# Kernel tuning notes

Measured on AMD Instinct MI355X. Metric: run time of the kernel, lower is better.

The kernel has to match this reference:

```python
import jax, jax.numpy as jnp
import numpy as np

B, L, D, C = 8, 4096, 1024, 64


def setup_inputs() -> dict:
    key = jax.random.key(0)
    ks = jax.random.split(key, 9)
    s = 1.0 / np.sqrt(D)

    def lin(k):
        kw, kb = jax.random.split(k)
        return (jax.random.uniform(kw, (D, D), jnp.float32, -s, s),
                jax.random.uniform(kb, (D,), jnp.float32, -s, s))

    Wq_w, Wq_b = lin(ks[1])
    Wk_w, Wk_b = lin(ks[2])
    Wv_w, Wv_b = lin(ks[3])
    Wo_w, Wo_b = lin(ks[4])
    return {
        "X": jax.random.normal(ks[0], (B, L, D), jnp.float32),
        "chunk": C,
        "Wq_w": Wq_w, "Wq_b": Wq_b,
        "Wk_w": Wk_w, "Wk_b": Wk_b,
        "Wv_w": Wv_w, "Wv_b": Wv_b,
        "Wo_w": Wo_w, "Wo_b": Wo_b,
    }


def _chunk_delta_rule(Q, K, V, beta, Cc):
    # Q,K,V: (B,L,d); beta: (B,L,1); Cc divides L
    Bq, Lq, d = Q.shape
    nc = Lq // Cc
    Q, K, V = (x.reshape(Bq, nc, Cc, d) for x in (Q, K, V))
    beta = beta.reshape(Bq, nc, Cc, 1)
    Kb = K * beta
    Vb = V * beta
    tril_strict = jnp.tril(jnp.ones((Cc, Cc), jnp.float32), -1)
    # masked_fill(triu(diag=0), 0) keeps strictly-lower part
    T = -(Kb @ jnp.swapaxes(K, -1, -2)) * tril_strict  # (B,nc,C,C)
    # forward-substitution inverse of (I - strict_lower); C is small & static
    for i in range(1, Cc):
        T = T.at[:, :, i, :i].add(
            jnp.einsum('bnj,bnjc->bnc', T[:, :, i, :], T[:, :, :, :i]))
    T = T + jnp.eye(Cc, dtype=T.dtype)
    W = T @ Kb  # (B,nc,C,d)
    U = T @ Vb  # (B,nc,C,d)
    tril_incl = jnp.tril(jnp.ones((Cc, Cc), jnp.float32))  # masked_fill(triu(1),0)

    def step(S, xs):
        q, k, w, u0 = xs  # each (B,C,d)
        u = u0 - w @ S
        A = (q @ jnp.swapaxes(k, -1, -2)) * tril_incl  # (B,C,C)
        o = A @ u + q @ S
        return S + jnp.swapaxes(k, -1, -2) @ u, o

    S0 = jnp.zeros((Bq, d, d), Q.dtype)
    xs = tuple(jnp.swapaxes(a, 0, 1) for a in (Q, K, W, U))  # (nc,B,C,d)
    _, O = jax.lax.scan(step, S0, xs)
    return jnp.swapaxes(O, 0, 1).reshape(Bq, Lq, d)


def reference(X, chunk, Wq_w, Wq_b, Wk_w, Wk_b, Wv_w, Wv_b, Wo_w, Wo_b):
    Q = X @ Wq_w.T + Wq_b
    K = X @ Wk_w.T + Wk_b
    V = X @ Wv_w.T + Wv_b
    beta = 1.0 / (jnp.sum(K * K, axis=-1, keepdims=True) + 1e-6)
    O = _chunk_delta_rule(Q, K, V, beta, chunk)
    return O @ Wo_w.T + Wo_b
```

## Files before the change

kernel.cpp:

```cpp
#include <hip/hip_runtime.h>
#include <stdint.h>

typedef unsigned short u16;
typedef __attribute__((ext_vector_type(8))) short short8;
typedef __attribute__((ext_vector_type(4))) float float4_;

#define NB 8
#define LL 4096
#define DD 1024
#define CC 64
#define NCH 64

__device__ __forceinline__ u16 f2bf(float f) {
  union { float f; uint32_t u; } v; v.f = f;
  uint32_t u = v.u;
  return (u16)((u + 0x7fffu + ((u >> 16) & 1u)) >> 16);
}
__device__ __forceinline__ float bf2f(u16 h) {
  union { uint32_t u; float f; } v; v.u = ((uint32_t)h) << 16;
  return v.f;
}
__device__ __forceinline__ float4_ mfma16(short8 a, short8 b, float4_ c) {
  return __builtin_amdgcn_mfma_f32_16x16x32_bf16(a, b, c, 0, 0, 0);
}

__global__ void k_detect(const uint32_t* __restrict__ X, int* __restrict__ flag) {
  if (threadIdx.x == 0 && blockIdx.x == 0) {
    int votes = 0;
    for (int i = 0; i < 64; ++i) {
      uint32_t w = X[i];
      uint32_t e = (w >> 7) & 0xFF;
      votes += (e > 134 || e < 110) ? 1 : 0;
    }
    *flag = (votes < 8) ? 1 : 0;
  }
}

__global__ __launch_bounds__(256) void k_convert(const void* __restrict__ src, u16* __restrict__ dst,
                                                 long n8, const int* __restrict__ flag) {
  long i = (long)blockIdx.x * 256 + threadIdx.x;
  if (i >= n8) return;
  if (*flag) {
    ((short8*)dst)[i] = ((const short8*)src)[i];
  } else {
    const float4_* s = (const float4_*)src;
    float4_ a = s[2 * i], b = s[2 * i + 1];
    short8 o;
#pragma unroll
    for (int j = 0; j < 4; ++j) { o[j] = (short)f2bf(a[j]); o[4 + j] = (short)f2bf(b[j]); }
    ((short8*)dst)[i] = o;
  }
}

template <bool DUAL>
__device__ __forceinline__ void gemm128(const u16* __restrict__ A, const u16* __restrict__ W,
                                        const u16* __restrict__ bias, void* __restrict__ Out,
                                        int m0, int n0, const int* __restrict__ flag) {
  __shared__ __attribute__((aligned(16))) u16 As[128 * 64];
  __shared__ __attribute__((aligned(16))) u16 Bs[128 * 64];
  const int tid = threadIdx.x, lane = tid & 63, wv = tid >> 6;
  float4_ acc[2][8];
#pragma unroll
  for (int i = 0; i < 2; ++i)
#pragma unroll
    for (int j = 0; j < 8; ++j) acc[i][j] = (float4_)0.f;

  for (int kk = 0; kk < DD; kk += 64) {
#pragma unroll
    for (int i = 0; i < 4; ++i) {
      int e = tid + 256 * i;
      int row = e >> 3, col = (e & 7) * 8;
      *(short8*)&As[row * 64 + col] = *(const short8*)(A + (size_t)(m0 + row) * DD + kk + col);
      *(short8*)&Bs[row * 64 + col] = *(const short8*)(W + (size_t)(n0 + row) * DD + kk + col);
    }
    __syncthreads();
#pragma unroll
    for (int ks = 0; ks < 2; ++ks) {
      short8 af[2];
#pragma unroll
      for (int mt = 0; mt < 2; ++mt)
        af[mt] = *(const short8*)&As[(32 * wv + 16 * mt + (lane & 15)) * 64 + ks * 32 + (lane >> 4) * 8];
#pragma unroll
      for (int nt = 0; nt < 8; ++nt) {
        short8 bf = *(const short8*)&Bs[(16 * nt + (lane & 15)) * 64 + ks * 32 + (lane >> 4) * 8];
#pragma unroll
        for (int mt = 0; mt < 2; ++mt) acc[mt][nt] = mfma16(af[mt], bf, acc[mt][nt]);
      }
    }
    __syncthreads();
  }
  const bool obf = DUAL ? (*flag != 0) : true;
#pragma unroll
  for (int mt = 0; mt < 2; ++mt)
#pragma unroll
    for (int nt = 0; nt < 8; ++nt) {
      int rg = m0 + 32 * wv + 16 * mt + ((lane >> 4) << 2);
      int cg = n0 + 16 * nt + (lane & 15);
      float bv = bf2f(bias[cg]);
#pragma unroll
      for (int r = 0; r < 4; ++r) {
        float o = acc[mt][nt][r] + bv;
        if (obf) ((u16*)Out)[(size_t)(rg + r) * DD + cg] = f2bf(o);
        else     ((float*)Out)[(size_t)(rg + r) * DD + cg] = o;
      }
    }
}

__global__ __launch_bounds__(256) void k_gemm_qkv(const u16* __restrict__ X,
    const u16* __restrict__ Wq, const u16* __restrict__ bq,
    const u16* __restrict__ Wk, const u16* __restrict__ bk,
    const u16* __restrict__ Wv, const u16* __restrict__ bv,
    u16* __restrict__ Qo, u16* __restrict__ Ko, u16* __restrict__ Vo) {
  int nb = blockIdx.x;
  int mat = nb >> 3, nt = nb & 7;
  const u16 *W, *bi; u16* O;
  if (mat == 0)      { W = Wq; bi = bq; O = Qo; }
  else if (mat == 1) { W = Wk; bi = bk; O = Ko; }
  else               { W = Wv; bi = bv; O = Vo; }
  gemm128<false>(X, W, bi, O, blockIdx.y * 128, nt * 128, nullptr);
}

__global__ __launch_bounds__(256) void k_gemm_o(const u16* __restrict__ A,
    const u16* __restrict__ Wo, const u16* __restrict__ bo, void* __restrict__ Out,
    const int* __restrict__ flag) {
  gemm128<true>(A, Wo, bo, Out, blockIdx.y * 128, blockIdx.x * 128, flag);
}

__global__ __launch_bounds__(256) void k_prep(const u16* __restrict__ Q, const u16* __restrict__ K,
                                              u16* __restrict__ V ,
                                              u16* __restrict__ Aout, u16* __restrict__ Wall,
                                              u16* __restrict__ KTg) {
  const int ch = blockIdx.x, b = blockIdx.y;
  const size_t row0 = (size_t)b * LL + (size_t)ch * CC;
  const int tid = threadIdx.x, lane = tid & 63, wv = tid >> 6;

  __shared__ __attribute__((aligned(16))) float Gs[64 * 65];
  __shared__ __attribute__((aligned(16))) float Ts[64 * 65];
  __shared__ __attribute__((aligned(16))) u16 Kt[64 * 64];
  __shared__ __attribute__((aligned(16))) u16 Qt[64 * 64];
  __shared__ __attribute__((aligned(16))) u16 T2s[64 * 72];
  __shared__ float betas[64];

  float4_ accG[4], accA[4];
#pragma unroll
  for (int ct = 0; ct < 4; ++ct) { accG[ct] = (float4_)0.f; accA[ct] = (float4_)0.f; }

  for (int kk = 0; kk < DD; kk += 64) {
#pragma unroll
    for (int i = 0; i < 2; ++i) {
      int e = tid + 256 * i;
      int row = e >> 3, col = (e & 7) * 8;
      *(short8*)&Kt[row * 64 + col] = *(const short8*)(K + (row0 + row) * DD + kk + col);
      *(short8*)&Qt[row * 64 + col] = *(const short8*)(Q + (row0 + row) * DD + kk + col);
    }
    __syncthreads();
#pragma unroll
    for (int ks = 0; ks < 2; ++ks) {
      short8 ak = *(const short8*)&Kt[(16 * wv + (lane & 15)) * 64 + ks * 32 + (lane >> 4) * 8];
      short8 aq = *(const short8*)&Qt[(16 * wv + (lane & 15)) * 64 + ks * 32 + (lane >> 4) * 8];
#pragma unroll
      for (int ct = 0; ct < 4; ++ct) {
        short8 bk = *(const short8*)&Kt[(16 * ct + (lane & 15)) * 64 + ks * 32 + (lane >> 4) * 8];
        accG[ct] = mfma16(ak, bk, accG[ct]);
        accA[ct] = mfma16(aq, bk, accA[ct]);
      }
    }
    __syncthreads();
  }
  u16* Abase = Aout + (size_t)(b * NCH + ch) * (CC * CC);
#pragma unroll
  for (int ct = 0; ct < 4; ++ct) {
    int i0 = 16 * wv + ((lane >> 4) << 2);
    int c = 16 * ct + (lane & 15);
#pragma unroll
    for (int r = 0; r < 4; ++r) {
      int i = i0 + r;
      Gs[i * 65 + c] = accG[ct][r];
      Abase[i * 64 + c] = f2bf((c <= i) ? accA[ct][r] : 0.f);
    }
  }
  __syncthreads();
  if (tid < 64) betas[tid] = 1.f / (Gs[tid * 65 + tid] + 1e-6f);
  __syncthreads();
  for (int e = tid; e < 4096; e += 256) {
    int i = e >> 6, c = e & 63;
    Ts[i * 65 + c] = (c < i) ? (-betas[i] * Gs[i * 65 + c]) : 0.f;
  }
  __syncthreads();
  for (int i = 1; i < 64; ++i) {
    float rv = 0.f, acc = 0.f;
    if (tid < 64) {
      rv = Ts[i * 65 + tid];
      for (int j = 1; j < i; ++j) {
        float a = __shfl(rv, j);
        acc += a * Ts[j * 65 + tid];
      }
    }
    __syncthreads();
    if (tid < i) Ts[i * 65 + tid] = rv + acc;
    __syncthreads();
  }
  if (tid < 64) Ts[tid * 65 + tid] += 1.f;
  __syncthreads();
  for (int e = tid; e < 4096; e += 256) {
    int i = e >> 6, j = e & 63;
    T2s[i * 72 + j] = f2bf(Ts[i * 65 + j] * betas[j]);
  }
  __syncthreads();

  u16* KTs = (u16*)Gs;
  u16* VTs = (u16*)Ts;
  for (int kk = 0; kk < DD; kk += 64) {
#pragma unroll
    for (int rep = 0; rep < 2; ++rep) {
      int t = tid >> 2;
      int c0 = (tid & 3) * 8 + rep * 32;
      short8 vv = *(const short8*)(V + (row0 + t) * DD + kk + c0);
      short8 vk = *(const short8*)(K + (row0 + t) * DD + kk + c0);
#pragma unroll
      for (int e = 0; e < 8; ++e) { VTs[(c0 + e) * 72 + t] = (u16)vv[e]; KTs[(c0 + e) * 72 + t] = (u16)vk[e]; }
    }
    __syncthreads();
#pragma unroll
    for (int w2 = 0; w2 < 2; ++w2) {
      int e = tid + 256 * w2;
      int jl = e >> 3, toff = (e & 7) * 8;
      *(short8*)(KTg + ((size_t)b * DD + kk + jl) * LL + (size_t)ch * CC + toff) =
          *(const short8*)&KTs[jl * 72 + toff];
    }
    float4_ accU[4], accW[4];
#pragma unroll
    for (int ct = 0; ct < 4; ++ct) { accU[ct] = (float4_)0.f; accW[ct] = (float4_)0.f; }
#pragma unroll
    for (int ks = 0; ks < 2; ++ks) {
      short8 a2 = *(const short8*)&T2s[(16 * wv + (lane & 15)) * 72 + ks * 32 + (lane >> 4) * 8];
#pragma unroll
      for (int ct = 0; ct < 4; ++ct) {
        short8 bu = *(const short8*)&VTs[(16 * ct + (lane & 15)) * 72 + ks * 32 + (lane >> 4) * 8];
        short8 bw = *(const short8*)&KTs[(16 * ct + (lane & 15)) * 72 + ks * 32 + (lane >> 4) * 8];
        accU[ct] = mfma16(a2, bu, accU[ct]);
        accW[ct] = mfma16(a2, bw, accW[ct]);
      }
    }
#pragma unroll
    for (int ct = 0; ct < 4; ++ct) {
      int i0 = 16 * wv + ((lane >> 4) << 2);
      int c = kk + 16 * ct + (lane & 15);
#pragma unroll
      for (int r = 0; r < 4; ++r) {
        V[(row0 + i0 + r) * DD + c]    = f2bf(accU[ct][r]);
        Wall[(row0 + i0 + r) * DD + c] = f2bf(accW[ct][r]);
      }
    }
    __syncthreads();
  }
}

__global__ __launch_bounds__(256, 1) void k_scan_fused(
    const u16* __restrict__ Q, const u16* __restrict__ Wg, const u16* __restrict__ KTg,
    const u16* __restrict__ U0, const u16* __restrict__ Ag, u16* __restrict__ Og) {
  __shared__ __attribute__((aligned(16))) float S[32 * 1028];
  __shared__ __attribute__((aligned(16))) float u_acc[64 * 33];
  __shared__ __attribute__((aligned(16))) float oq_acc[64 * 33];
  __shared__ __attribute__((aligned(16))) u16 uT[32 * 72];

  const int b = blockIdx.x & 7;
  const int dc0 = (blockIdx.x >> 3) * 32;
  const int tid = threadIdx.x, lane = tid & 63, wv = tid >> 6;
  const int r15 = lane & 15, hi = lane >> 4;
  const int khi = hi * 8;
  const int tI = tid >> 2, cI = (tid & 3) * 8;

  for (int i = tid; i < 32 * 1028; i += 256) S[i] = 0.f;
  __syncthreads();

  for (int ch = 0; ch < NCH; ++ch) {
    const size_t row0 = (size_t)b * LL + (size_t)ch * CC;
    {
      short8 v = *(const short8*)(U0 + (row0 + tI) * DD + dc0 + cI);
#pragma unroll
      for (int e = 0; e < 8; ++e) {
        u_acc[tI * 33 + cI + e]  = bf2f((u16)v[e]);
        oq_acc[tI * 33 + cI + e] = 0.f;
      }
    }
    __syncthreads();
    {
      float4_ up[4][2], qp[4][2];
#pragma unroll
      for (int tt = 0; tt < 4; ++tt)
#pragma unroll
        for (int dt = 0; dt < 2; ++dt) { up[tt][dt] = (float4_)0.f; qp[tt][dt] = (float4_)0.f; }
#pragma unroll 2
      for (int ks = 0; ks < 8; ++ks) {
        const int j0 = wv * 256 + ks * 32 + khi;
        short8 sf[2];
#pragma unroll
        for (int dt = 0; dt < 2; ++dt) {
          const float* sp = &S[(dt * 16 + r15) * 1028 + j0];
          float4_ x0 = *(const float4_*)sp;
          float4_ x1 = *(const float4_*)(sp + 4);
          short8 s;
#pragma unroll
          for (int e = 0; e < 4; ++e) { s[e] = (short)f2bf(x0[e]); s[4 + e] = (short)f2bf(x1[e]); }
          sf[dt] = s;
        }
#pragma unroll
        for (int tt = 0; tt < 4; ++tt) {
          const size_t rbase = (row0 + tt * 16 + r15) * DD + j0;
          short8 wf = *(const short8*)(Wg + rbase);
          short8 qf = *(const short8*)(Q + rbase);
#pragma unroll
          for (int dt = 0; dt < 2; ++dt) {
            up[tt][dt] = mfma16(wf, sf[dt], up[tt][dt]);
            qp[tt][dt] = mfma16(qf, sf[dt], qp[tt][dt]);
          }
        }
      }
#pragma unroll
      for (int tt = 0; tt < 4; ++tt)
#pragma unroll
        for (int dt = 0; dt < 2; ++dt) {
          const int t0 = tt * 16 + hi * 4, dc = dt * 16 + r15;
#pragma unroll
          for (int r = 0; r < 4; ++r) {
            atomicAdd(&u_acc[(t0 + r) * 33 + dc], -up[tt][dt][r]);
            atomicAdd(&oq_acc[(t0 + r) * 33 + dc], qp[tt][dt][r]);
          }
        }
    }
    __syncthreads();
    {
      const float* pu = &u_acc[tI * 33 + cI];
#pragma unroll
      for (int e = 0; e < 8; ++e) uT[(cI + e) * 72 + tI] = f2bf(pu[e]);
    }
    __syncthreads();
    {
      short8 ub[2][2];
#pragma unroll
      for (int dt = 0; dt < 2; ++dt)
#pragma unroll
        for (int ks = 0; ks < 2; ++ks)
          ub[dt][ks] = *(const short8*)&uT[(dt * 16 + r15) * 72 + ks * 32 + khi];
      const size_t ktb = ((size_t)b * DD) * LL + (size_t)ch * CC;
#pragma unroll 4
      for (int djt = 0; djt < 16; ++djt) {
        const int dj0 = wv * 256 + djt * 16;
        short8 kf0 = *(const short8*)(KTg + ktb + (size_t)(dj0 + r15) * LL + khi);
        short8 kf1 = *(const short8*)(KTg + ktb + (size_t)(dj0 + r15) * LL + 32 + khi);
#pragma unroll
        for (int dt = 0; dt < 2; ++dt) {
          float* sp = &S[(dt * 16 + r15) * 1028 + dj0 + hi * 4];
          float4_ c = *(const float4_*)sp;
          c = mfma16(kf0, ub[dt][0], c);
          c = mfma16(kf1, ub[dt][1], c);
          *(float4_*)sp = c;
        }
      }
      const u16* Ab = Ag + (size_t)(b * NCH + ch) * (CC * CC);
      short8 af0 = *(const short8*)(Ab + (wv * 16 + r15) * CC + khi);
      short8 af1 = *(const short8*)(Ab + (wv * 16 + r15) * CC + 32 + khi);
      const int t0 = wv * 16 + hi * 4;
#pragma unroll
      for (int dt = 0; dt < 2; ++dt) {
        const int dc = dt * 16 + r15;
        float4_ c;
#pragma unroll
        for (int r = 0; r < 4; ++r) c[r] = oq_acc[(t0 + r) * 33 + dc];
        c = mfma16(af0, ub[dt][0], c);
        c = mfma16(af1, ub[dt][1], c);
#pragma unroll
        for (int r = 0; r < 4; ++r)
          Og[(row0 + t0 + r) * DD + dc0 + dc] = f2bf(c[r]);
      }
    }
    __syncthreads();
  }
}

extern "C" void kernel_launch(void* const* d_in, const int* in_sizes, int n_in,
                              void* d_out, int out_size, void* d_ws, size_t ws_size,
                              hipStream_t stream) {
  (void)in_sizes; (void)n_in; (void)out_size; (void)ws_size;
  const void* X  = d_in[0];
  const void* Wq = d_in[2]; const void* bq = d_in[3];
  const void* Wk = d_in[4]; const void* bk = d_in[5];
  const void* Wv = d_in[6]; const void* bv = d_in[7];
  const void* Wo = d_in[8]; const void* bo = d_in[9];

  char* ws = (char*)d_ws;
  int* flag = (int*)ws;
  char* p = ws + 256;
  const size_t E2 = (size_t)NB * LL * DD * 2;
  u16* xb   = (u16*)p; p += E2;
  u16* kt   = xb;
  u16* wqb  = (u16*)p; p += (size_t)DD * DD * 2;
  u16* wkb  = (u16*)p; p += (size_t)DD * DD * 2;
  u16* wvb  = (u16*)p; p += (size_t)DD * DD * 2;
  u16* wob  = (u16*)p; p += (size_t)DD * DD * 2;
  u16* bqb  = (u16*)p; p += 4096;
  u16* bkb  = (u16*)p; p += 4096;
  u16* bvb  = (u16*)p; p += 4096;
  u16* bob  = (u16*)p; p += 4096;
  u16* q_ws = (u16*)p; p += E2;
  u16* k_ws = (u16*)p; p += E2;
  u16* v_ws = (u16*)p; p += E2;
  u16* a_ws = (u16*)p; p += (size_t)NB * NCH * CC * CC * 2;
  u16* w_all = (u16*)p; p += E2;

  k_detect<<<1, 64, 0, stream>>>((const uint32_t*)X, flag);
  const long nX = (long)NB * LL * DD / 8;
  k_convert<<<(nX + 255) / 256, 256, 0, stream>>>(X, xb, nX, flag);
  const long nW = (long)DD * DD / 8;
  k_convert<<<(nW + 255) / 256, 256, 0, stream>>>(Wq, wqb, nW, flag);
  k_convert<<<(nW + 255) / 256, 256, 0, stream>>>(Wk, wkb, nW, flag);
  k_convert<<<(nW + 255) / 256, 256, 0, stream>>>(Wv, wvb, nW, flag);
  k_convert<<<(nW + 255) / 256, 256, 0, stream>>>(Wo, wob, nW, flag);
  const long nBias = DD / 8;
  k_convert<<<1, 256, 0, stream>>>(bq, bqb, nBias, flag);
  k_convert<<<1, 256, 0, stream>>>(bk, bkb, nBias, flag);
  k_convert<<<1, 256, 0, stream>>>(bv, bvb, nBias, flag);
  k_convert<<<1, 256, 0, stream>>>(bo, bob, nBias, flag);

  k_gemm_qkv<<<dim3(24, 256), 256, 0, stream>>>(xb, wqb, bqb, wkb, bkb, wvb, bvb, q_ws, k_ws, v_ws);
  k_prep<<<dim3(64, 8), 256, 0, stream>>>(q_ws, k_ws, v_ws, a_ws, w_all, kt);
  k_scan_fused<<<dim3(256), 256, 0, stream>>>(q_ws, w_all, kt, v_ws, a_ws, k_ws);
  k_gemm_o<<<dim3(8, 256), 256, 0, stream>>>(k_ws, wob, bob, d_out, flag);
}
```

Measured before the change: 3.022 ms.

## Double scan block threads, remove uT transpose staging, prefetch next chunk U0

The fused chunk scan kernel now runs 512 threads (8 waves) per block, so each wave handles half the d-range for the S·W/Q products and the S update. The u transpose now goes straight from u_acc into registers with packed bf16 conversion instructions, which removes the uT shared buffer. The next chunk's U0 load and the oq_acc reset are folded into the end of the previous iteration, dropping one barrier per chunk. The output A·u step is split across 8 waves, one tile each. The aim is more latency hiding in the serial scan, at the cost of more register pressure under the 512-thread launch bound and more shared-memory atomic contention.

```diff
diff --git a/kernel.cpp b/kernel.cpp
--- a/kernel.cpp
+++ b/kernel.cpp
@@ -4,6 +4,7 @@
 typedef unsigned short u16;
 typedef __attribute__((ext_vector_type(8))) short short8;
 typedef __attribute__((ext_vector_type(4))) float float4_;
+typedef __attribute__((ext_vector_type(4))) unsigned short us4;
 
 #define NB 8
 #define LL 4096
@@ -23,6 +24,12 @@
 __device__ __forceinline__ float4_ mfma16(short8 a, short8 b, float4_ c) {
   return __builtin_amdgcn_mfma_f32_16x16x32_bf16(a, b, c, 0, 0, 0);
 }
+__device__ __forceinline__ uint32_t cvtpk(float lo, float hi) {
+  uint32_t r;
+  asm("v_cvt_pk_bf16_f32 %0, %1, %2" : "=v"(r) : "v"(lo), "v"(hi));
+  return r;
+}
+union S8U { short8 s; uint32_t w[4]; };
 
 __global__ void k_detect(const uint32_t* __restrict__ X, int* __restrict__ flag) {
   if (threadIdx.x == 0 && blockIdx.x == 0) {
@@ -256,54 +263,54 @@
   }
 }
 
-__global__ __launch_bounds__(256, 1) void k_scan_fused(
+__global__ __launch_bounds__(512, 2) void k_scan_fused(
     const u16* __restrict__ Q, const u16* __restrict__ Wg, const u16* __restrict__ KTg,
     const u16* __restrict__ U0, const u16* __restrict__ Ag, u16* __restrict__ Og) {
   __shared__ __attribute__((aligned(16))) float S[32 * 1028];
   __shared__ __attribute__((aligned(16))) float u_acc[64 * 33];
   __shared__ __attribute__((aligned(16))) float oq_acc[64 * 33];
-  __shared__ __attribute__((aligned(16))) u16 uT[32 * 72];
 
   const int b = blockIdx.x & 7;
   const int dc0 = (blockIdx.x >> 3) * 32;
   const int tid = threadIdx.x, lane = tid & 63, wv = tid >> 6;
   const int r15 = lane & 15, hi = lane >> 4;
   const int khi = hi * 8;
-  const int tI = tid >> 2, cI = (tid & 3) * 8;
-
-  for (int i = tid; i < 32 * 1028; i += 256) S[i] = 0.f;
+  const int tIq = tid >> 3, cIq = (tid & 7) * 4;
+
+  for (int i = tid; i < 32 * 1028; i += 512) S[i] = 0.f;
+  {
+    us4 v = *(const us4*)(U0 + ((size_t)b * LL + tIq) * DD + dc0 + cIq);
+#pragma unroll
+    for (int e = 0; e < 4; ++e) {
+      u_acc[tIq * 33 + cIq + e] = bf2f(v[e]);
+      oq_acc[tIq * 33 + cIq + e] = 0.f;
+    }
+  }
   __syncthreads();
 
   for (int ch = 0; ch < NCH; ++ch) {
     const size_t row0 = (size_t)b * LL + (size_t)ch * CC;
     {
-      short8 v = *(const short8*)(U0 + (row0 + tI) * DD + dc0 + cI);
-#pragma unroll
-      for (int e = 0; e < 8; ++e) {
-        u_acc[tI * 33 + cI + e]  = bf2f((u16)v[e]);
-        oq_acc[tI * 33 + cI + e] = 0.f;
-      }
-    }
-    __syncthreads();
-    {
       float4_ up[4][2], qp[4][2];
 #pragma unroll
       for (int tt = 0; tt < 4; ++tt)
 #pragma unroll
         for (int dt = 0; dt < 2; ++dt) { up[tt][dt] = (float4_)0.f; qp[tt][dt] = (float4_)0.f; }
-#pragma unroll 2
-      for (int ks = 0; ks < 8; ++ks) {
-        const int j0 = wv * 256 + ks * 32 + khi;
+#pragma unroll
+      for (int ks = 0; ks < 4; ++ks) {
+        const int j0 = wv * 128 + ks * 32 + khi;
         short8 sf[2];
 #pragma unroll
         for (int dt = 0; dt < 2; ++dt) {
           const float* sp = &S[(dt * 16 + r15) * 1028 + j0];
           float4_ x0 = *(const float4_*)sp;
           float4_ x1 = *(const float4_*)(sp + 4);
-          short8 s;
-#pragma unroll
-          for (int e = 0; e < 4; ++e) { s[e] = (short)f2bf(x0[e]); s[4 + e] = (short)f2bf(x1[e]); }
-          sf[dt] = s;
+          S8U u;
+          u.w[0] = cvtpk(x0[0], x0[1]);
+          u.w[1] = cvtpk(x0[2], x0[3]);
+          u.w[2] = cvtpk(x1[0], x1[1]);
+          u.w[3] = cvtpk(x1[2], x1[3]);
+          sf[dt] = u.s;
         }
 #pragma unroll
         for (int tt = 0; tt < 4; ++tt) {
@@ -330,23 +337,28 @@
         }
     }
     __syncthreads();
+    short8 ub[2][2];
+#pragma unroll
+    for (int dt = 0; dt < 2; ++dt) {
+      const int dc = dt * 16 + r15;
+#pragma unroll
+      for (int ks = 0; ks < 2; ++ks) {
+        S8U u;
+#pragma unroll
+        for (int w2 = 0; w2 < 4; ++w2) {
+          float lo = u_acc[(ks * 32 + khi + 2 * w2) * 33 + dc];
+          float hi2 = u_acc[(ks * 32 + khi + 2 * w2 + 1) * 33 + dc];
+          u.w[w2] = cvtpk(lo, hi2);
+        }
+        ub[dt][ks] = u.s;
+      }
+    }
+    __syncthreads();
     {
-      const float* pu = &u_acc[tI * 33 + cI];
-#pragma unroll
-      for (int e = 0; e < 8; ++e) uT[(cI + e) * 72 + tI] = f2bf(pu[e]);
-    }
-    __syncthreads();
-    {
-      short8 ub[2][2];
-#pragma unroll
-      for (int dt = 0; dt < 2; ++dt)
-#pragma unroll
-        for (int ks = 0; ks < 2; ++ks)
-          ub[dt][ks] = *(const short8*)&uT[(dt * 16 + r15) * 72 + ks * 32 + khi];
       const size_t ktb = ((size_t)b * DD) * LL + (size_t)ch * CC;
 #pragma unroll 4
-      for (int djt = 0; djt < 16; ++djt) {
-        const int dj0 = wv * 256 + djt * 16;
+      for (int djt = 0; djt < 8; ++djt) {
+        const int dj0 = wv * 128 + djt * 16;
         short8 kf0 = *(const short8*)(KTg + ktb + (size_t)(dj0 + r15) * LL + khi);
         short8 kf1 = *(const short8*)(KTg + ktb + (size_t)(dj0 + r15) * LL + 32 + khi);
 #pragma unroll
@@ -358,21 +370,24 @@
           *(float4_*)sp = c;
         }
       }
+      const int tt = wv & 3, dtw = wv >> 2;
       const u16* Ab = Ag + (size_t)(b * NCH + ch) * (CC * CC);
-      short8 af0 = *(const short8*)(Ab + (wv * 16 + r15) * CC + khi);
-      short8 af1 = *(const short8*)(Ab + (wv * 16 + r15) * CC + 32 + khi);
-      const int t0 = wv * 16 + hi * 4;
-#pragma unroll
-      for (int dt = 0; dt < 2; ++dt) {
-        const int dc = dt * 16 + r15;
-        float4_ c;
-#pragma unroll
-        for (int r = 0; r < 4; ++r) c[r] = oq_acc[(t0 + r) * 33 + dc];
-        c = mfma16(af0, ub[dt][0], c);
-        c = mfma16(af1, ub[dt][1], c);
-#pragma unroll
-        for (int r = 0; r < 4; ++r)
-          Og[(row0 + t0 + r) * DD + dc0 + dc] = f2bf(c[r]);
+      short8 af0 = *(const short8*)(Ab + (tt * 16 + r15) * CC + khi);
+      short8 af1 = *(const short8*)(Ab + (tt * 16 + r15) * CC + 32 + khi);
+      const int t0 = tt * 16 + hi * 4;
+      const int dc = dtw * 16 + r15;
+      float4_ c;
+#pragma unroll
+      for (int r = 0; r < 4; ++r) { c[r] = oq_acc[(t0 + r) * 33 + dc]; oq_acc[(t0 + r) * 33 + dc] = 0.f; }
+      c = mfma16(af0, ub[dtw][0], c);
+      c = mfma16(af1, ub[dtw][1], c);
+#pragma unroll
+      for (int r = 0; r < 4; ++r)
+        Og[(row0 + t0 + r) * DD + dc0 + dc] = f2bf(c[r]);
+      if (ch + 1 < NCH) {
+        us4 v = *(const us4*)(U0 + (row0 + CC + tIq) * DD + dc0 + cIq);
+#pragma unroll
+        for (int e = 0; e < 4; ++e) u_acc[tIq * 33 + cIq + e] = bf2f(v[e]);
       }
     }
     __syncthreads();
@@ -425,6 +440,6 @@
 
   k_gemm_qkv<<<dim3(24, 256), 256, 0, stream>>>(xb, wqb, bqb, wkb, bkb, wvb, bvb, q_ws, k_ws, v_ws);
   k_prep<<<dim3(64, 8), 256, 0, stream>>>(q_ws, k_ws, v_ws, a_ws, w_all, kt);
-  k_scan_fused<<<dim3(256), 256, 0, stream>>>(q_ws, w_all, kt, v_ws, a_ws, k_ws);
+  k_scan_fused<<<dim3(256), 512, 0, stream>>>(q_ws, w_all, kt, v_ws, a_ws, k_ws);
   k_gemm_o<<<dim3(8, 256), 256, 0, stream>>>(k_ws, wob, bob, d_out, flag);
 }
```

After: 4.397 ms. 1.45x slower.

## Tile Q/W/KT into contiguous 64x64 blocks and pipeline scan loads via LDS

Applied to the files above, without the earlier changes.

Q, W and K-transpose are now written in per-chunk 64x64 tiled layouts so the scan kernel can stream them with global_load_lds into a triple-buffered, XOR-swizzled LDS staging ring. The S@W/S@Q contraction is restructured so each wave owns rows and accumulates in registers over the full d dimension, which removes the LDS atomicAdd reductions and the u_acc/oq_acc buffers. Packed bf16 conversion instructions replace the scalar rounding, and the output overwrites the V buffer. The cost is more complex index math and tighter waitcnt/barrier synchronization, and each chunk now runs through longer serial loops with one barrier per step.

```diff
diff --git a/kernel.cpp b/kernel.cpp
--- a/kernel.cpp
+++ b/kernel.cpp
@@ -22,6 +22,18 @@
 }
 __device__ __forceinline__ float4_ mfma16(short8 a, short8 b, float4_ c) {
   return __builtin_amdgcn_mfma_f32_16x16x32_bf16(a, b, c, 0, 0, 0);
+}
+__device__ __forceinline__ uint32_t cvtpk(float lo, float hi) {
+  uint32_t r;
+  asm("v_cvt_pk_bf16_f32 %0, %1, %2" : "=v"(r) : "v"(lo), "v"(hi));
+  return r;
+}
+union S8U { short8 s; uint32_t w[4]; };
+
+__device__ __forceinline__ void gld_lds16(const u16* g, u16* l) {
+  __builtin_amdgcn_global_load_lds(
+      (const __attribute__((address_space(1))) uint32_t*)g,
+      (__attribute__((address_space(3))) uint32_t*)l, 16, 0, 0);
 }
 
 __global__ void k_detect(const uint32_t* __restrict__ X, int* __restrict__ flag) {
@@ -52,7 +64,7 @@
   }
 }
 
-template <bool DUAL>
+template <int OM>
 __device__ __forceinline__ void gemm128(const u16* __restrict__ A, const u16* __restrict__ W,
                                         const u16* __restrict__ bias, void* __restrict__ Out,
                                         int m0, int n0, const int* __restrict__ flag) {
@@ -89,7 +101,7 @@
     }
     __syncthreads();
   }
-  const bool obf = DUAL ? (*flag != 0) : true;
+  const bool obf = (OM == 1) ? (*flag != 0) : true;
 #pragma unroll
   for (int mt = 0; mt < 2; ++mt)
 #pragma unroll
@@ -100,8 +112,17 @@
 #pragma unroll
       for (int r = 0; r < 4; ++r) {
         float o = acc[mt][nt][r] + bv;
-        if (obf) ((u16*)Out)[(size_t)(rg + r) * DD + cg] = f2bf(o);
-        else     ((float*)Out)[(size_t)(rg + r) * DD + cg] = o;
+        if (OM == 2) {
+          int row = rg + r;
+          int bb = row >> 12, l = row & 4095;
+          size_t dst = ((size_t)((bb * 64 + (l >> 6)) * 16 + (cg >> 6))) * 4096 +
+                       (size_t)(l & 63) * 64 + (cg & 63);
+          ((u16*)Out)[dst] = f2bf(o);
+        } else if (obf) {
+          ((u16*)Out)[(size_t)(rg + r) * DD + cg] = f2bf(o);
+        } else {
+          ((float*)Out)[(size_t)(rg + r) * DD + cg] = o;
+        }
       }
     }
 }
@@ -110,26 +131,24 @@
     const u16* __restrict__ Wq, const u16* __restrict__ bq,
     const u16* __restrict__ Wk, const u16* __restrict__ bk,
     const u16* __restrict__ Wv, const u16* __restrict__ bv,
-    u16* __restrict__ Qo, u16* __restrict__ Ko, u16* __restrict__ Vo) {
+    u16* __restrict__ Qo , u16* __restrict__ Ko, u16* __restrict__ Vo) {
   int nb = blockIdx.x;
   int mat = nb >> 3, nt = nb & 7;
-  const u16 *W, *bi; u16* O;
-  if (mat == 0)      { W = Wq; bi = bq; O = Qo; }
-  else if (mat == 1) { W = Wk; bi = bk; O = Ko; }
-  else               { W = Wv; bi = bv; O = Vo; }
-  gemm128<false>(X, W, bi, O, blockIdx.y * 128, nt * 128, nullptr);
+  if (mat == 0)      gemm128<2>(X, Wq, bq, Qo, blockIdx.y * 128, nt * 128, nullptr);
+  else if (mat == 1) gemm128<0>(X, Wk, bk, Ko, blockIdx.y * 128, nt * 128, nullptr);
+  else               gemm128<0>(X, Wv, bv, Vo, blockIdx.y * 128, nt * 128, nullptr);
 }
 
 __global__ __launch_bounds__(256) void k_gemm_o(const u16* __restrict__ A,
     const u16* __restrict__ Wo, const u16* __restrict__ bo, void* __restrict__ Out,
     const int* __restrict__ flag) {
-  gemm128<true>(A, Wo, bo, Out, blockIdx.y * 128, blockIdx.x * 128, flag);
-}
-
-__global__ __launch_bounds__(256) void k_prep(const u16* __restrict__ Q, const u16* __restrict__ K,
+  gemm128<1>(A, Wo, bo, Out, blockIdx.y * 128, blockIdx.x * 128, flag);
+}
+
+__global__ __launch_bounds__(256) void k_prep(const u16* __restrict__ Qtl, const u16* __restrict__ K,
                                               u16* __restrict__ V ,
-                                              u16* __restrict__ Aout, u16* __restrict__ Wall,
-                                              u16* __restrict__ KTg) {
+                                              u16* __restrict__ Aout, u16* __restrict__ Wt,
+                                              u16* __restrict__ KTt) {
   const int ch = blockIdx.x, b = blockIdx.y;
   const size_t row0 = (size_t)b * LL + (size_t)ch * CC;
   const int tid = threadIdx.x, lane = tid & 63, wv = tid >> 6;
@@ -146,12 +165,13 @@
   for (int ct = 0; ct < 4; ++ct) { accG[ct] = (float4_)0.f; accA[ct] = (float4_)0.f; }
 
   for (int kk = 0; kk < DD; kk += 64) {
+    const size_t qtb = ((size_t)(b * NCH + ch) * 16 + (kk >> 6)) * 4096;
 #pragma unroll
     for (int i = 0; i < 2; ++i) {
       int e = tid + 256 * i;
       int row = e >> 3, col = (e & 7) * 8;
       *(short8*)&Kt[row * 64 + col] = *(const short8*)(K + (row0 + row) * DD + kk + col);
-      *(short8*)&Qt[row * 64 + col] = *(const short8*)(Q + (row0 + row) * DD + kk + col);
+      *(short8*)&Qt[e * 8] = *(const short8*)(Qtl + qtb + (size_t)e * 8);
     }
     __syncthreads();
 #pragma unroll
@@ -211,6 +231,7 @@
   u16* KTs = (u16*)Gs;
   u16* VTs = (u16*)Ts;
   for (int kk = 0; kk < DD; kk += 64) {
+    const size_t tlb = ((size_t)(b * NCH + ch) * 16 + (kk >> 6)) * 4096;
 #pragma unroll
     for (int rep = 0; rep < 2; ++rep) {
       int t = tid >> 2;
@@ -225,8 +246,7 @@
     for (int w2 = 0; w2 < 2; ++w2) {
       int e = tid + 256 * w2;
       int jl = e >> 3, toff = (e & 7) * 8;
-      *(short8*)(KTg + ((size_t)b * DD + kk + jl) * LL + (size_t)ch * CC + toff) =
-          *(const short8*)&KTs[jl * 72 + toff];
+      *(short8*)(KTt + tlb + (size_t)jl * 64 + toff) = *(const short8*)&KTs[jl * 72 + toff];
     }
     float4_ accU[4], accW[4];
 #pragma unroll
@@ -245,11 +265,11 @@
 #pragma unroll
     for (int ct = 0; ct < 4; ++ct) {
       int i0 = 16 * wv + ((lane >> 4) << 2);
-      int c = kk + 16 * ct + (lane & 15);
+      int cl = 16 * ct + (lane & 15);
 #pragma unroll
       for (int r = 0; r < 4; ++r) {
-        V[(row0 + i0 + r) * DD + c]    = f2bf(accU[ct][r]);
-        Wall[(row0 + i0 + r) * DD + c] = f2bf(accW[ct][r]);
+        V[(row0 + i0 + r) * DD + kk + cl] = f2bf(accU[ct][r]);
+        Wt[tlb + (size_t)(i0 + r) * 64 + cl] = f2bf(accW[ct][r]);
       }
     }
     __syncthreads();
@@ -257,123 +277,171 @@
 }
 
 __global__ __launch_bounds__(256, 1) void k_scan_fused(
-    const u16* __restrict__ Q, const u16* __restrict__ Wg, const u16* __restrict__ KTg,
-    const u16* __restrict__ U0, const u16* __restrict__ Ag, u16* __restrict__ Og) {
+    const u16* __restrict__ Qt, const u16* __restrict__ Wt, const u16* __restrict__ KTt,
+    u16* __restrict__ U0 , const u16* __restrict__ Ag) {
   __shared__ __attribute__((aligned(16))) float S[32 * 1028];
-  __shared__ __attribute__((aligned(16))) float u_acc[64 * 33];
-  __shared__ __attribute__((aligned(16))) float oq_acc[64 * 33];
+  __shared__ __attribute__((aligned(16))) u16 stg[3 * 4096];
   __shared__ __attribute__((aligned(16))) u16 uT[32 * 72];
 
   const int b = blockIdx.x & 7;
   const int dc0 = (blockIdx.x >> 3) * 32;
   const int tid = threadIdx.x, lane = tid & 63, wv = tid >> 6;
   const int r15 = lane & 15, hi = lane >> 4;
-  const int khi = hi * 8;
-  const int tI = tid >> 2, cI = (tid & 3) * 8;
+  const int arow = 16 * wv + r15;
+  const int aoff = arow * 32 + ((hi ^ ((arow >> 1) & 3)) << 3);
+  const int koff0 = arow * 64 + ((hi ^ (arow & 7)) << 3);
+  const int koff1 = arow * 64 + (((4 + hi) ^ (arow & 7)) << 3);
+  const int tC = 16 * wv + hi * 4;
+  const int s_row = tid >> 2;
+  const int s_src = s_row * 64 + (((tid & 3) ^ ((s_row >> 1) & 3)) << 3);
+  const int l1 = tid + 256;
+  const int k_src0 = (tid >> 3) * 64 + (((tid & 7) ^ ((tid >> 3) & 7)) << 3);
+  const int k_src1 = (l1 >> 3) * 64 + (((l1 & 7) ^ ((l1 >> 3) & 7)) << 3);
+  u16* wdst = &stg[wv * 512];
 
   for (int i = tid; i < 32 * 1028; i += 256) S[i] = 0.f;
   __syncthreads();
 
   for (int ch = 0; ch < NCH; ++ch) {
     const size_t row0 = (size_t)b * LL + (size_t)ch * CC;
+    const size_t tb = (size_t)(b * NCH + ch) * 16;
+
+    u16 u0r[2][4];
+#pragma unroll
+    for (int dt = 0; dt < 2; ++dt)
+#pragma unroll
+      for (int r = 0; r < 4; ++r)
+        u0r[dt][r] = U0[(row0 + tC + r) * DD + dc0 + dt * 16 + r15];
+
+    float4_ uacc[2], oqa[2];
+    uacc[0] = (float4_)0.f; uacc[1] = (float4_)0.f;
+    oqa[0] = (float4_)0.f;  oqa[1] = (float4_)0.f;
+
+    auto issue1 = [&](int hs) {
+      const int s = hs >> 1, ks = (hs & 1) * 32, slot = hs % 3;
+      gld_lds16(Wt + (tb + s) * 4096 + ks + s_src, wdst + slot * 4096);
+      gld_lds16(Qt + (tb + s) * 4096 + ks + s_src, wdst + slot * 4096 + 2048);
+    };
+    issue1(0); issue1(1);
+
+#pragma unroll 1
+    for (int hs = 0; hs < 31; ++hs) {
+      asm volatile("s_waitcnt vmcnt(2)" ::: "memory");
+      __builtin_amdgcn_s_barrier();
+      __builtin_amdgcn_sched_barrier(0);
+      if (hs + 2 < 32) issue1(hs + 2);
+      const int slot = hs % 3;
+      const u16* wb = &stg[slot * 4096];
+      short8 afw = *(const short8*)&wb[aoff];
+      short8 afq = *(const short8*)&wb[2048 + aoff];
+      const int jb = hs * 32 + hi * 8;
+#pragma unroll
+      for (int dt = 0; dt < 2; ++dt) {
+        const float* sp = &S[(dt * 16 + r15) * 1028 + jb];
+        float4_ x0 = *(const float4_*)sp;
+        float4_ x1 = *(const float4_*)(sp + 4);
+        S8U u;
+        u.w[0] = cvtpk(x0[0], x0[1]); u.w[1] = cvtpk(x0[2], x0[3]);
+        u.w[2] = cvtpk(x1[0], x1[1]); u.w[3] = cvtpk(x1[2], x1[3]);
+        uacc[dt] = mfma16(afw, u.s, uacc[dt]);
+        oqa[dt]  = mfma16(afq, u.s, oqa[dt]);
+      }
+    }
     {
-      short8 v = *(const short8*)(U0 + (row0 + tI) * DD + dc0 + cI);
-#pragma unroll
-      for (int e = 0; e < 8; ++e) {
-        u_acc[tI * 33 + cI + e]  = bf2f((u16)v[e]);
-        oq_acc[tI * 33 + cI + e] = 0.f;
-      }
-    }
-    __syncthreads();
+      asm volatile("s_waitcnt vmcnt(0)" ::: "memory");
+      __builtin_amdgcn_s_barrier();
+      __builtin_amdgcn_sched_barrier(0);
+      const int slot = 31 % 3;
+      const u16* wb = &stg[slot * 4096];
+      short8 afw = *(const short8*)&wb[aoff];
+      short8 afq = *(const short8*)&wb[2048 + aoff];
+      const int jb = 31 * 32 + hi * 8;
+#pragma unroll
+      for (int dt = 0; dt < 2; ++dt) {
+        const float* sp = &S[(dt * 16 + r15) * 1028 + jb];
+        float4_ x0 = *(const float4_*)sp;
+        float4_ x1 = *(const float4_*)(sp + 4);
+        S8U u;
+        u.w[0] = cvtpk(x0[0], x0[1]); u.w[1] = cvtpk(x0[2], x0[3]);
+        u.w[2] = cvtpk(x1[0], x1[1]); u.w[3] = cvtpk(x1[2], x1[3]);
+        uacc[dt] = mfma16(afw, u.s, uacc[dt]);
+        oqa[dt]  = mfma16(afq, u.s, oqa[dt]);
+      }
+    }
+#pragma unroll
+    for (int dt = 0; dt < 2; ++dt) {
+      float v0 = bf2f(u0r[dt][0]) - uacc[dt][0];
+      float v1 = bf2f(u0r[dt][1]) - uacc[dt][1];
+      float v2 = bf2f(u0r[dt][2]) - uacc[dt][2];
+      float v3 = bf2f(u0r[dt][3]) - uacc[dt][3];
+      uint32_t* d = (uint32_t*)&uT[(dt * 16 + r15) * 72 + tC];
+      d[0] = cvtpk(v0, v1);
+      d[1] = cvtpk(v2, v3);
+    }
+    __syncthreads();
+
+    short8 ub[2][2];
+#pragma unroll
+    for (int dt = 0; dt < 2; ++dt)
+#pragma unroll
+      for (int ks = 0; ks < 2; ++ks)
+        ub[dt][ks] = *(const short8*)&uT[(dt * 16 + r15) * 72 + ks * 32 + hi * 8];
+    const u16* Ab = Ag + (size_t)(b * NCH + ch) * (CC * CC);
+    short8 afA0 = *(const short8*)(Ab + arow * 64 + hi * 8);
+    short8 afA1 = *(const short8*)(Ab + arow * 64 + 32 + hi * 8);
+
+    auto issue3 = [&](int ts) {
+      const int slot = ts % 3;
+      gld_lds16(KTt + (tb + ts) * 4096 + k_src0, wdst + slot * 4096);
+      gld_lds16(KTt + (tb + ts) * 4096 + k_src1, wdst + slot * 4096 + 2048);
+    };
+    issue3(0); issue3(1);
+
+#pragma unroll 1
+    for (int ts = 0; ts < 15; ++ts) {
+      asm volatile("s_waitcnt vmcnt(2)" ::: "memory");
+      __builtin_amdgcn_s_barrier();
+      __builtin_amdgcn_sched_barrier(0);
+      if (ts + 2 < 16) issue3(ts + 2);
+      const int slot = ts % 3;
+      const u16* kb = &stg[slot * 4096];
+      short8 kf0 = *(const short8*)&kb[koff0];
+      short8 kf1 = *(const short8*)&kb[koff1];
+#pragma unroll
+      for (int dt = 0; dt < 2; ++dt) {
+        float* sp = &S[(dt * 16 + r15) * 1028 + ts * 64 + wv * 16 + hi * 4];
+        float4_ c = *(const float4_*)sp;
+        c = mfma16(kf0, ub[dt][0], c);
+        c = mfma16(kf1, ub[dt][1], c);
+        *(float4_*)sp = c;
+      }
+    }
     {
-      float4_ up[4][2], qp[4][2];
-#pragma unroll
-      for (int tt = 0; tt < 4; ++tt)
-#pragma unroll
-        for (int dt = 0; dt < 2; ++dt) { up[tt][dt] = (float4_)0.f; qp[tt][dt] = (float4_)0.f; }
-#pragma unroll 2
-      for (int ks = 0; ks < 8; ++ks) {
-        const int j0 = wv * 256 + ks * 32 + khi;
-        short8 sf[2];
-#pragma unroll
-        for (int dt = 0; dt < 2; ++dt) {
-          const float* sp = &S[(dt * 16 + r15) * 1028 + j0];
-          float4_ x0 = *(const float4_*)sp;
-          float4_ x1 = *(const float4_*)(sp + 4);
-          short8 s;
-#pragma unroll
-          for (int e = 0; e < 4; ++e) { s[e] = (short)f2bf(x0[e]); s[4 + e] = (short)f2bf(x1[e]); }
-          sf[dt] = s;
-        }
-#pragma unroll
-        for (int tt = 0; tt < 4; ++tt) {
-          const size_t rbase = (row0 + tt * 16 + r15) * DD + j0;
-          short8 wf = *(const short8*)(Wg + rbase);
-          short8 qf = *(const short8*)(Q + rbase);
-#pragma unroll
-          for (int dt = 0; dt < 2; ++dt) {
-            up[tt][dt] = mfma16(wf, sf[dt], up[tt][dt]);
-            qp[tt][dt] = mfma16(qf, sf[dt], qp[tt][dt]);
-          }
-        }
-      }
-#pragma unroll
-      for (int tt = 0; tt < 4; ++tt)
-#pragma unroll
-        for (int dt = 0; dt < 2; ++dt) {
-          const int t0 = tt * 16 + hi * 4, dc = dt * 16 + r15;
-#pragma unroll
-          for (int r = 0; r < 4; ++r) {
-            atomicAdd(&u_acc[(t0 + r) * 33 + dc], -up[tt][dt][r]);
-            atomicAdd(&oq_acc[(t0 + r) * 33 + dc], qp[tt][dt][r]);
-          }
-        }
-    }
-    __syncthreads();
-    {
-      const float* pu = &u_acc[tI * 33 + cI];
-#pragma unroll
-      for (int e = 0; e < 8; ++e) uT[(cI + e) * 72 + tI] = f2bf(pu[e]);
-    }
-    __syncthreads();
-    {
-      short8 ub[2][2];
-#pragma unroll
-      for (int dt = 0; dt < 2; ++dt)
-#pragma unroll
-        for (int ks = 0; ks < 2; ++ks)
-          ub[dt][ks] = *(const short8*)&uT[(dt * 16 + r15) * 72 + ks * 32 + khi];
-      const size_t ktb = ((size_t)b * DD) * LL + (size_t)ch * CC;
-#pragma unroll 4
-      for (int djt = 0; djt < 16; ++djt) {
-        const int dj0 = wv * 256 + djt * 16;
-        short8 kf0 = *(const short8*)(KTg + ktb + (size_t)(dj0 + r15) * LL + khi);
-        short8 kf1 = *(const short8*)(KTg + ktb + (size_t)(dj0 + r15) * LL + 32 + khi);
-#pragma unroll
-        for (int dt = 0; dt < 2; ++dt) {
-          float* sp = &S[(dt * 16 + r15) * 1028 + dj0 + hi * 4];
-          float4_ c = *(const float4_*)sp;
-          c = mfma16(kf0, ub[dt][0], c);
-          c = mfma16(kf1, ub[dt][1], c);
-          *(float4_*)sp = c;
-        }
-      }
-      const u16* Ab = Ag + (size_t)(b * NCH + ch) * (CC * CC);
-      short8 af0 = *(const short8*)(Ab + (wv * 16 + r15) * CC + khi);
-      short8 af1 = *(const short8*)(Ab + (wv * 16 + r15) * CC + 32 + khi);
-      const int t0 = wv * 16 + hi * 4;
+      asm volatile("s_waitcnt vmcnt(0)" ::: "memory");
+      __builtin_amdgcn_s_barrier();
+      __builtin_amdgcn_sched_barrier(0);
+      const u16* kb = &stg[(15 % 3) * 4096];
+      short8 kf0 = *(const short8*)&kb[koff0];
+      short8 kf1 = *(const short8*)&kb[koff1];
 #pragma unroll
       for (int dt = 0; dt < 2; ++dt) {
-        const int dc = dt * 16 + r15;
-        float4_ c;
-#pragma unroll
-        for (int r = 0; r < 4; ++r) c[r] = oq_acc[(t0 + r) * 33 + dc];
-        c = mfma16(af0, ub[dt][0], c);
-        c = mfma16(af1, ub[dt][1], c);
-#pragma unroll
-        for (int r = 0; r < 4; ++r)
-          Og[(row0 + t0 + r) * DD + dc0 + dc] = f2bf(c[r]);
-      }
+        float* sp = &S[(dt * 16 + r15) * 1028 + 15 * 64 + wv * 16 + hi * 4];
+        float4_ c = *(const float4_*)sp;
+        c = mfma16(kf0, ub[dt][0], c);
+        c = mfma16(kf1, ub[dt][1], c);
+        *(float4_*)sp = c;
+      }
+    }
+#pragma unroll
+    for (int dt = 0; dt < 2; ++dt) {
+      float4_ c;
+#pragma unroll
+      for (int r = 0; r < 4; ++r) c[r] = oqa[dt][r];
+      c = mfma16(afA0, ub[dt][0], c);
+      c = mfma16(afA1, ub[dt][1], c);
+#pragma unroll
+      for (int r = 0; r < 4; ++r)
+        U0[(row0 + tC + r) * DD + dc0 + dt * 16 + r15] = f2bf(c[r]);
     }
     __syncthreads();
   }
@@ -394,7 +462,7 @@
   char* p = ws + 256;
   const size_t E2 = (size_t)NB * LL * DD * 2;
   u16* xb   = (u16*)p; p += E2;
-  u16* kt   = xb;
+  u16* ktt  = xb;
   u16* wqb  = (u16*)p; p += (size_t)DD * DD * 2;
   u16* wkb  = (u16*)p; p += (size_t)DD * DD * 2;
   u16* wvb  = (u16*)p; p += (size_t)DD * DD * 2;
@@ -403,11 +471,11 @@
   u16* bkb  = (u16*)p; p += 4096;
   u16* bvb  = (u16*)p; p += 4096;
   u16* bob  = (u16*)p; p += 4096;
-  u16* q_ws = (u16*)p; p += E2;
+  u16* q_tl = (u16*)p; p += E2;
   u16* k_ws = (u16*)p; p += E2;
   u16* v_ws = (u16*)p; p += E2;
   u16* a_ws = (u16*)p; p += (size_t)NB * NCH * CC * CC * 2;
-  u16* w_all = (u16*)p; p += E2;
+  u16* w_tl = (u16*)p; p += E2;
 
   k_detect<<<1, 64, 0, stream>>>((const uint32_t*)X, flag);
   const long nX = (long)NB * LL * DD / 8;
@@ -423,8 +491,8 @@
   k_convert<<<1, 256, 0, stream>>>(bv, bvb, nBias, flag);
   k_convert<<<1, 256, 0, stream>>>(bo, bob, nBias, flag);
 
-  k_gemm_qkv<<<dim3(24, 256), 256, 0, stream>>>(xb, wqb, bqb, wkb, bkb, wvb, bvb, q_ws, k_ws, v_ws);
-  k_prep<<<dim3(64, 8), 256, 0, stream>>>(q_ws, k_ws, v_ws, a_ws, w_all, kt);
-  k_scan_fused<<<dim3(256), 256, 0, stream>>>(q_ws, w_all, kt, v_ws, a_ws, k_ws);
-  k_gemm_o<<<dim3(8, 256), 256, 0, stream>>>(k_ws, wob, bob, d_out, flag);
-}
+  k_gemm_qkv<<<dim3(24, 256), 256, 0, stream>>>(xb, wqb, bqb, wkb, bkb, wvb, bvb, q_tl, k_ws, v_ws);
+  k_prep<<<dim3(64, 8), 256, 0, stream>>>(q_tl, k_ws, v_ws, a_ws, w_tl, ktt);
+  k_scan_fused<<<dim3(256), 256, 0, stream>>>(q_tl, w_tl, ktt, v_ws, a_ws);
+  k_gemm_o<<<dim3(8, 256), 256, 0, stream>>>(v_ws, wob, bob, d_out, flag);
+}
```

Result: faster. 2.604 ms (-13.8%).
